# Kernel tuning notes

Hardware: AMD Instinct MI355X
Metric: run time of the kernel (lower is better)

The kernel has to match this reference:

```python
import jax, jax.numpy as jnp
import numpy as np

N_EMBD = 1024
N_HEAD = 16
EPS = 1e-5


def setup_inputs() -> dict:
    key = jax.random.key(0)
    ks = jax.random.split(key, 12)
    C = N_EMBD
    s = 1.0 / np.sqrt(C)
    s4 = 1.0 / np.sqrt(4 * C)
    return {
        "x": jax.random.normal(ks[0], (2, 2048, C), jnp.float32),
        # attention projections (stored as [in, out])
        "wq": jax.random.normal(ks[1], (C, C), jnp.float32) * s,
        "bq": jnp.zeros((C,), jnp.float32),
        "wk": jax.random.normal(ks[2], (C, C), jnp.float32) * s,
        "bk": jnp.zeros((C,), jnp.float32),
        "wv": jax.random.normal(ks[3], (C, C), jnp.float32) * s,
        "bv": jnp.zeros((C,), jnp.float32),
        # layernorms
        "ln1_w": jnp.ones((C,), jnp.float32),
        "ln1_b": jnp.zeros((C,), jnp.float32),
        "ln2_w": jnp.ones((C,), jnp.float32),
        "ln2_b": jnp.zeros((C,), jnp.float32),
        # MLP
        "w_fc": jax.random.normal(ks[4], (C, 4 * C), jnp.float32) * s,
        "b_fc": jnp.zeros((4 * C,), jnp.float32),
        "w_proj": jax.random.normal(ks[5], (4 * C, C), jnp.float32) * s4,
        "b_proj": jnp.zeros((C,), jnp.float32),
    }


def _layer_norm(x, w, b):
    mu = jnp.mean(x, axis=-1, keepdims=True)
    var = jnp.var(x, axis=-1, keepdims=True)
    return (x - mu) * jax.lax.rsqrt(var + EPS) * w + b


def _block(x, wq, bq, wk, bk, wv, bv, ln1_w, ln1_b, ln2_w, ln2_b,
           w_fc, b_fc, w_proj, b_proj):
    B, T, C = x.shape
    H, D = N_HEAD, C // N_HEAD
    h = _layer_norm(x, ln1_w, ln1_b)
    q = (h @ wq + bq).reshape(B, T, H, D).transpose(0, 2, 1, 3)  # [B,H,T,D]
    k = (h @ wk + bk).reshape(B, T, H, D).transpose(0, 2, 1, 3)
    v = (h @ wv + bv).reshape(B, T, H, D).transpose(0, 2, 1, 3)
    att = jnp.einsum("bhtd,bhsd->bhts", q, k) / np.sqrt(D)
    causal = jnp.tril(jnp.ones((T, T), bool))
    att = jnp.where(causal, att, -jnp.inf)
    att = jax.nn.softmax(att, axis=-1)
    y = jnp.einsum("bhts,bhsd->bhtd", att, v)
    y = y.transpose(0, 2, 1, 3).reshape(B, T, C)
    x = x + y
    h2 = _layer_norm(x, ln2_w, ln2_b)
    mlp = jax.nn.gelu(h2 @ w_fc + b_fc, approximate=False) @ w_proj + b_proj
    x = x + mlp
    return x, k, v


def reference(x, wq, bq, wk, bk, wv, bv, ln1_w, ln1_b, ln2_w, ln2_b,
              w_fc, b_fc, w_proj, b_proj):
    return _block(x, wq, bq, wk, bk, wv, bv, ln1_w, ln1_b, ln2_w, ln2_b,
                  w_fc, b_fc, w_proj, b_proj)
```

## Files before the change

### kernel.cpp

```cpp
#include <hip/hip_runtime.h>
#include <hip/hip_bf16.h>


#define T_SEQ 2048
#define C_DIM 1024
#define HEADS 16
#define HD    64

typedef __attribute__((ext_vector_type(8))) short s16x8;
typedef __attribute__((ext_vector_type(4))) short s16x4;
typedef __attribute__((ext_vector_type(4))) float f32x4;

__device__ __forceinline__ short f2bf(float f) {
    union { __hip_bfloat16 h; short s; } u;
    u.h = __float2bfloat16(f);
    return u.s;
}
__device__ __forceinline__ float bf2f(short s) {
    union { float f; unsigned u; } u;
    u.u = ((unsigned)(unsigned short)s) << 16;
    return u.f;
}

__device__ __forceinline__ void gload16(const void* g, void* l) {
    __builtin_amdgcn_global_load_lds(
        (const __attribute__((address_space(1))) void*)g,
        (__attribute__((address_space(3))) void*)l, 16, 0, 0);
}
#define VMCNT0 asm volatile("s_waitcnt vmcnt(0)" ::: "memory")
#define PRIO1  __builtin_amdgcn_s_setprio(1)
#define PRIO0  __builtin_amdgcn_s_setprio(0)

__global__ __launch_bounds__(256) void prep_kernel(
    const float* __restrict__ wq, const float* __restrict__ wk, const float* __restrict__ wv,
    const float* __restrict__ wfc, const float* __restrict__ wpr,
    short* __restrict__ wqkvt, short* __restrict__ wfct, short* __restrict__ wprt,
    const float* __restrict__ x, const float* __restrict__ ln1w, const float* __restrict__ ln1b,
    short* __restrict__ hb) {
    int b = blockIdx.x, tid = threadIdx.x;
    if (b < 11264) {
        const float* W; short* Wt; int K, N, n0, k0;
        if (b < 3072) {
            int which = b >> 10, sub = b & 1023;
            W = (which == 0) ? wq : ((which == 1) ? wk : wv);
            Wt = wqkvt + which * 1024 * 1024;
            K = 1024; N = 1024;
            n0 = (sub & 31) * 32; k0 = (sub >> 5) * 32;
        } else if (b < 7168) {
            int sub = b - 3072;
            W = wfc; Wt = wfct; K = 1024; N = 4096;
            n0 = (sub & 127) * 32; k0 = (sub >> 7) * 32;
        } else {
            int sub = b - 7168;
            W = wpr; Wt = wprt; K = 4096; N = 1024;
            n0 = (sub & 31) * 32; k0 = (sub >> 5) * 32;
        }
        __shared__ float t[32][33];
        int ty = tid >> 3, tx = tid & 7;
        float4 v = *(const float4*)&W[(size_t)(k0 + ty) * N + n0 + tx * 4];
        t[ty][tx * 4 + 0] = v.x; t[ty][tx * 4 + 1] = v.y;
        t[ty][tx * 4 + 2] = v.z; t[ty][tx * 4 + 3] = v.w;
        __syncthreads();
        int r = tid >> 3, c = tid & 7;
        s16x4 o;
#pragma unroll
        for (int j = 0; j < 4; j++) o[j] = f2bf(t[c * 4 + j][r]);
        *(s16x4*)&Wt[(size_t)(n0 + r) * K + k0 + c * 4] = o;
    } else {
        int row = b - 11264;
        float4 v = ((const float4*)(x + (size_t)row * C_DIM))[tid];
        float s  = v.x + v.y + v.z + v.w;
        float sq = v.x * v.x + v.y * v.y + v.z * v.z + v.w * v.w;
#pragma unroll
        for (int off = 32; off > 0; off >>= 1) {
            s  += __shfl_down(s, off, 64);
            sq += __shfl_down(sq, off, 64);
        }
        __shared__ float rs[4], rq[4];
        int wv2 = tid >> 6, ln = tid & 63;
        if (ln == 0) { rs[wv2] = s; rq[wv2] = sq; }
        __syncthreads();
        s = rs[0] + rs[1] + rs[2] + rs[3];
        sq = rq[0] + rq[1] + rq[2] + rq[3];
        float mean = s * (1.f / C_DIM);
        float rstd = rsqrtf(sq * (1.f / C_DIM) - mean * mean + 1e-5f);
        float4 wv4 = ((const float4*)ln1w)[tid];
        float4 bv4 = ((const float4*)ln1b)[tid];
        s16x4 o;
        o[0] = f2bf((v.x - mean) * rstd * wv4.x + bv4.x);
        o[1] = f2bf((v.y - mean) * rstd * wv4.y + bv4.y);
        o[2] = f2bf((v.z - mean) * rstd * wv4.z + bv4.z);
        o[3] = f2bf((v.w - mean) * rstd * wv4.w + bv4.w);
        *(s16x4*)(hb + (size_t)row * C_DIM + tid * 4) = o;
    }
}

__global__ __launch_bounds__(256) void resln_kernel(
    const float* __restrict__ x, const float* __restrict__ y,
    const float* __restrict__ w, const float* __restrict__ b,
    const float* __restrict__ bproj,
    short* __restrict__ out, float* __restrict__ xout) {
    int row = blockIdx.x, tid = threadIdx.x;
    float4 vx = ((const float4*)(x + row * C_DIM))[tid];
    float4 vy = ((const float4*)(y + row * C_DIM))[tid];
    float4 v;
    v.x = vx.x + vy.x; v.y = vx.y + vy.y; v.z = vx.z + vy.z; v.w = vx.w + vy.w;
    float4 bp = ((const float4*)bproj)[tid];
    float4 xo;
    xo.x = v.x + bp.x; xo.y = v.y + bp.y; xo.z = v.z + bp.z; xo.w = v.w + bp.w;
    ((float4*)(xout + row * C_DIM))[tid] = xo;
    float s  = v.x + v.y + v.z + v.w;
    float sq = v.x * v.x + v.y * v.y + v.z * v.z + v.w * v.w;
#pragma unroll
    for (int off = 32; off > 0; off >>= 1) {
        s  += __shfl_down(s, off, 64);
        sq += __shfl_down(sq, off, 64);
    }
    __shared__ float rs[4], rq[4];
    int wv = tid >> 6, ln = tid & 63;
    if (ln == 0) { rs[wv] = s; rq[wv] = sq; }
    __syncthreads();
    s = rs[0] + rs[1] + rs[2] + rs[3];
    sq = rq[0] + rq[1] + rq[2] + rq[3];
    float mean = s * (1.f / C_DIM);
    float rstd = rsqrtf(sq * (1.f / C_DIM) - mean * mean + 1e-5f);
    float4 wv4 = ((const float4*)w)[tid];
    float4 bv4 = ((const float4*)b)[tid];
    s16x4 o;
    o[0] = f2bf((v.x - mean) * rstd * wv4.x + bv4.x);
    o[1] = f2bf((v.y - mean) * rstd * wv4.y + bv4.y);
    o[2] = f2bf((v.z - mean) * rstd * wv4.z + bv4.z);
    o[3] = f2bf((v.w - mean) * rstd * wv4.w + bv4.w);
    *(s16x4*)(out + row * C_DIM + tid * 4) = o;
}

__global__ __launch_bounds__(256) void reduce_kernel(
    const short* __restrict__ p, float* __restrict__ xout) {
    size_t i = (size_t)blockIdx.x * 256 + threadIdx.x;
    float4 a = ((const float4*)xout)[i];
#pragma unroll
    for (int c = 0; c < 4; c++) {
        s16x4 v = ((const s16x4*)(p + (size_t)c * 4194304))[i];
        a.x += bf2f(v[0]); a.y += bf2f(v[1]); a.z += bf2f(v[2]); a.w += bf2f(v[3]);
    }
    ((float4*)xout)[i] = a;
}

template<int MODE>
__global__ __launch_bounds__(256, 3) void gemm97(
    const short* __restrict__ A, const short* __restrict__ Bt,
    int K, int LDA, int N,
    const float* __restrict__ b0, const float* __restrict__ b1, const float* __restrict__ b2,
    short* __restrict__ os0, short* __restrict__ os1, short* __restrict__ os2,
    float* __restrict__ of0) {
    __shared__ short As[128 * 64];
    __shared__ short Bs[128 * 64];
    const int tid = threadIdx.x;
    const int wv = tid >> 6, lane = tid & 63, g = lane >> 4, r4 = lane & 15;
    const int wr = wv >> 1, wc = wv & 1;
    const int lr = lane >> 3, lc = lane & 7, sc = lc ^ lr;

    const int nwg = gridDim.x * gridDim.y;
    const int bid = blockIdx.y * gridDim.x + blockIdx.x;
    const int swz = (bid & 7) * (nwg >> 3) + (bid >> 3);
    const int m0 = (swz % gridDim.x) * 128;
    const int yy = swz / gridDim.x;
    int n0, kch;
    if constexpr (MODE == 2) {
        kch = yy >> 3;
        n0 = (yy & 7) * 128;
    } else {
        kch = 0;
        n0 = yy * 128;
    }
    const size_t kbase = (size_t)kch * K;
    const size_t aoff = (size_t)m0 * LDA + kbase + sc * 8;
    const size_t boff = (size_t)n0 * LDA + kbase + sc * 8;

    const f32x4 zero4 = {0.f, 0.f, 0.f, 0.f};
    f32x4 acc[4][4];
#pragma unroll
    for (int i = 0; i < 4; i++)
#pragma unroll
        for (int j = 0; j < 4; j++) acc[i][j] = zero4;

    auto stage = [&](int t1) {
#pragma unroll
        for (int j = 0; j < 4; j++) {
            int rg = wv * 4 + j;
            gload16(A  + aoff + (size_t)(rg * 8 + lr) * LDA + (size_t)t1 * 64, &As[rg * 512]);
            gload16(Bt + boff + (size_t)(rg * 8 + lr) * LDA + (size_t)t1 * 64, &Bs[rg * 512]);
        }
    };

    stage(0);
    VMCNT0;
    __syncthreads();

    const int NT = K >> 6;
    for (int t = 0; t < NT; ++t) {
#pragma unroll
        for (int kk = 0; kk < 2; kk++) {
            s16x8 af[4], bfr[4];
#pragma unroll
            for (int mf = 0; mf < 4; mf++) {
                int row = wr * 64 + mf * 16 + r4;
                af[mf] = *(const s16x8*)((const char*)As +
                          ((row * 128 + kk * 64 + g * 16) ^ ((row & 7) << 4)));
            }
#pragma unroll
            for (int nf = 0; nf < 4; nf++) {
                int row = wc * 64 + nf * 16 + r4;
                bfr[nf] = *(const s16x8*)((const char*)Bs +
                           ((row * 128 + kk * 64 + g * 16) ^ ((row & 7) << 4)));
            }
#pragma unroll
            for (int mf = 0; mf < 4; mf++)
#pragma unroll
                for (int nf = 0; nf < 4; nf++)
                    acc[mf][nf] = __builtin_amdgcn_mfma_f32_16x16x32_bf16(
                        af[mf], bfr[nf], acc[mf][nf], 0, 0, 0);
        }
        __syncthreads();
        if (t + 1 < NT) stage(t + 1);
        VMCNT0;
        __syncthreads();
    }

#pragma unroll
    for (int mf = 0; mf < 4; mf++) {
#pragma unroll
        for (int nf = 0; nf < 4; nf++) {
            int n = n0 + wc * 64 + nf * 16 + r4;
            int mB = m0 + wr * 64 + mf * 16 + 4 * g;
            if constexpr (MODE == 0) {
                int sel = n >> 10, nn = n & 1023;
                const float* bp = (sel == 0) ? b0 : ((sel == 1) ? b1 : b2);
                float bias = bp[nn];
                int h = nn >> 6, d = nn & 63;
                int bb2 = mB >> 11, tt = mB & 2047;
                size_t qz = ((size_t)(bb2 * HEADS + h) * T_SEQ + tt) * HD + d;
                if (sel == 0) {
#pragma unroll
                    for (int r = 0; r < 4; r++) os0[qz + (size_t)r * HD] = f2bf(acc[mf][nf][r] + bias);
                } else if (sel == 1) {
#pragma unroll
                    for (int r = 0; r < 4; r++) {
                        float val = acc[mf][nf][r] + bias;
                        os1[qz + (size_t)r * HD] = f2bf(val);
                        of0[qz + (size_t)r * HD] = val;
                    }
                } else {
                    s16x4 vp;
#pragma unroll
                    for (int r = 0; r < 4; r++) {
                        float val = acc[mf][nf][r] + bias;
                        of0[4194304 + qz + (size_t)r * HD] = val;
                        vp[r] = f2bf(val);
                    }
                    *(s16x4*)&os2[((size_t)(bb2 * HEADS + h) * HD + d) * T_SEQ + tt] = vp;
                }
            } else if constexpr (MODE == 1) {
                float bias = b0[n];
#pragma unroll
                for (int r = 0; r < 4; r++) {
                    float val = acc[mf][nf][r] + bias;
                    val = 0.5f * val * (1.f + erff(val * 0.70710678118f));
                    os0[(size_t)(mB + r) * N + n] = f2bf(val);
                }
            } else {
#pragma unroll
                for (int r = 0; r < 4; r++)
                    os0[(size_t)kch * 4194304 + (size_t)(mB + r) * N + n] = f2bf(acc[mf][nf][r]);
            }
        }
    }
}

__global__ __launch_bounds__(256) void attn_kernel(
    const short* __restrict__ qb, const short* __restrict__ kb,
    const short* __restrict__ vtb, float* __restrict__ y) {
    __shared__ short Ks[2][64 * 64];
    __shared__ short Vs[2][64 * 64];
    __shared__ short Ps[4][16 * 64];
    int bx = blockIdx.x, bh = blockIdx.y;
    int tid = threadIdx.x, w = tid >> 6, lane = tid & 63, g = lane >> 4, r4 = lane & 15;
    int lr = lane >> 3, lc = lane & 7, sc = lc ^ lr;
    const float S2 = 0.125f * 1.44269504089f;
    const f32x4 zero4 = {0.f, 0.f, 0.f, 0.f};

    for (int ph = 0; ph < 2; ++ph) {
        int qtr = ph ? bx : (31 - bx);
        int qbase = qtr * 64;
        int nst = qtr + 1;

        const short* Qp = qb + ((size_t)bh * T_SEQ + qbase + w * 16 + r4) * HD;
        s16x8 qf0 = *(const s16x8*)&Qp[g * 8];
        s16x8 qf1 = *(const s16x8*)&Qp[32 + g * 8];

        f32x4 yacc[4];
#pragma unroll
        for (int ni = 0; ni < 4; ni++) yacc[ni] = zero4;
        float mrun = -1e30f, lrun = 0.f;

#pragma unroll
        for (int j = 0; j < 2; j++) {
            int rw = (w * 2 + j) * 8 + lr;
            gload16(kb  + ((size_t)bh * T_SEQ + rw) * HD + sc * 8, &Ks[0][(w * 2 + j) * 512]);
            gload16(vtb + ((size_t)bh * HD + rw) * T_SEQ + sc * 8, &Vs[0][(w * 2 + j) * 512]);
        }
        VMCNT0;
        __syncthreads();

        for (int st = 0; st < nst; ++st) {
            int cur = st & 1;
            int s0 = st * 64;
            if (st + 1 < nst) {
#pragma unroll
                for (int j = 0; j < 2; j++) {
                    int rw = (w * 2 + j) * 8 + lr;
                    gload16(kb  + ((size_t)bh * T_SEQ + s0 + 64 + rw) * HD + sc * 8,
                            &Ks[cur ^ 1][(w * 2 + j) * 512]);
                    gload16(vtb + ((size_t)bh * HD + rw) * T_SEQ + s0 + 64 + sc * 8,
                            &Vs[cur ^ 1][(w * 2 + j) * 512]);
                }
            }
            f32x4 sacc[4];
#pragma unroll
            for (int sb = 0; sb < 4; sb++) sacc[sb] = zero4;
            PRIO1;
#pragma unroll
            for (int kk = 0; kk < 2; kk++) {
                s16x8 qf = (kk == 0) ? qf0 : qf1;
#pragma unroll
                for (int sb = 0; sb < 4; sb++) {
                    int srow = sb * 16 + r4;
                    s16x8 kf = *(const s16x8*)((const char*)&Ks[cur][0] +
                                ((srow * 128 + kk * 64 + g * 16) ^ ((r4 & 7) << 4)));
                    sacc[sb] = __builtin_amdgcn_mfma_f32_16x16x32_bf16(kf, qf, sacc[sb], 0, 0, 0);
                }
            }
            PRIO0;
            bool diag = (st == qtr);
            float p[4][4];
            float mx = -1e30f;
#pragma unroll
            for (int sb = 0; sb < 4; sb++)
#pragma unroll
                for (int r = 0; r < 4; r++) {
                    float v = sacc[sb][r] * S2;
                    if (diag) {
                        int kv = s0 + sb * 16 + 4 * g + r;
                        int qg = qbase + w * 16 + r4;
                        if (kv > qg) v = -1e30f;
                    }
                    p[sb][r] = v;
                    mx = fmaxf(mx, v);
                }
            mx = fmaxf(mx, __shfl_xor(mx, 16, 64));
            mx = fmaxf(mx, __shfl_xor(mx, 32, 64));
            if (!__all(mx <= mrun + 8.f)) {
                float mnew = fmaxf(mrun, mx);
                float alpha = exp2f(mrun - mnew);
                float aC[4];
#pragma unroll
                for (int r = 0; r < 4; r++) aC[r] = __shfl(alpha, 4 * g + r, 64);
#pragma unroll
                for (int ni = 0; ni < 4; ni++)
#pragma unroll
                    for (int r = 0; r < 4; r++) yacc[ni][r] *= aC[r];
                lrun *= alpha;
                mrun = mnew;
            }
            float rsum = 0.f;
#pragma unroll
            for (int sb = 0; sb < 4; sb++)
#pragma unroll
                for (int r = 0; r < 4; r++) {
                    float e = exp2f(p[sb][r] - mrun);
                    p[sb][r] = e;
                    rsum += e;
                }
            rsum += __shfl_xor(rsum, 16, 64);
            rsum += __shfl_xor(rsum, 32, 64);
            lrun += rsum;
#pragma unroll
            for (int sb = 0; sb < 4; sb++) {
                s16x4 pk;
#pragma unroll
                for (int r = 0; r < 4; r++) pk[r] = f2bf(p[sb][r]);
                int off = (r4 * 128 + (sb * 16 + 4 * g) * 2) ^ ((r4 & 7) << 4);
                *(s16x4*)((char*)&Ps[w][0] + off) = pk;
            }
            PRIO1;
#pragma unroll
            for (int kk = 0; kk < 2; kk++) {
                s16x8 pf = *(const s16x8*)((const char*)&Ps[w][0] +
                            ((r4 * 128 + kk * 64 + g * 16) ^ ((r4 & 7) << 4)));
#pragma unroll
                for (int ni = 0; ni < 4; ni++) {
                    int vrow = ni * 16 + r4;
                    s16x8 vb = *(const s16x8*)((const char*)&Vs[cur][0] +
                                ((vrow * 128 + kk * 64 + g * 16) ^ ((r4 & 7) << 4)));
                    yacc[ni] = __builtin_amdgcn_mfma_f32_16x16x32_bf16(pf, vb, yacc[ni], 0, 0, 0);
                }
            }
            PRIO0;
            VMCNT0;
            __syncthreads();
        }
        float lC[4];
#pragma unroll
        for (int r = 0; r < 4; r++) lC[r] = __shfl(lrun, 4 * g + r, 64);
        int bb = bh >> 4, h = bh & 15;
#pragma unroll
        for (int ni = 0; ni < 4; ni++)
#pragma unroll
            for (int r = 0; r < 4; r++) {
                int q = qbase + w * 16 + 4 * g + r;
                y[((size_t)bb * T_SEQ + q) * C_DIM + h * HD + ni * 16 + r4] = yacc[ni][r] / lC[r];
            }
        __syncthreads();
    }
}

extern "C" void kernel_launch(void* const* d_in, const int* in_sizes, int n_in,
                              void* d_out, int out_size, void* d_ws, size_t ws_size,
                              hipStream_t stream) {
    (void)in_sizes; (void)n_in; (void)out_size; (void)ws_size;
    const float* x    = (const float*)d_in[0];
    const float* wq   = (const float*)d_in[1];
    const float* bq   = (const float*)d_in[2];
    const float* wk   = (const float*)d_in[3];
    const float* bk   = (const float*)d_in[4];
    const float* wvp  = (const float*)d_in[5];
    const float* bv   = (const float*)d_in[6];
    const float* ln1w = (const float*)d_in[7];
    const float* ln1b = (const float*)d_in[8];
    const float* ln2w = (const float*)d_in[9];
    const float* ln2b = (const float*)d_in[10];
    const float* wfc  = (const float*)d_in[11];
    const float* bfc  = (const float*)d_in[12];
    const float* wpr  = (const float*)d_in[13];
    const float* bpr  = (const float*)d_in[14];

    float* xout = (float*)d_out;
    float* kout = xout + 4194304;

    short* wqkvt = (short*)d_ws;
    short* wfct  = wqkvt + 3072 * 1024;
    short* wprt  = wfct + 4096 * 1024;
    short* hb    = wprt + 1024 * 4096;
    short* qb    = hb + 4096 * 1024;
    short* kbuf  = qb + 4096 * 1024;
    short* vtb   = kbuf + 4096 * 1024;
    short* h2b   = vtb + 4096 * 1024;
    short* fcb   = h2b + 4096 * 1024;
    float* ybuf  = (float*)(fcb + 4096 * 4096);
    short* pbuf  = qb;

    prep_kernel<<<15360, 256, 0, stream>>>(wq, wk, wvp, wfc, wpr,
        wqkvt, wfct, wprt, x, ln1w, ln1b, hb);

    gemm97<0><<<dim3(32, 24), 256, 0, stream>>>(hb, wqkvt, 1024, 1024, 3072,
        bq, bk, bv, qb, kbuf, vtb, kout);

    attn_kernel<<<dim3(16, 32), 256, 0, stream>>>(qb, kbuf, vtb, ybuf);

    resln_kernel<<<4096, 256, 0, stream>>>(x, ybuf, ln2w, ln2b, bpr, h2b, xout);

    gemm97<1><<<dim3(32, 32), 256, 0, stream>>>(h2b, wfct, 1024, 1024, 4096,
        bfc, nullptr, nullptr, fcb, nullptr, nullptr, nullptr);

    gemm97<2><<<dim3(32, 32), 256, 0, stream>>>(fcb, wprt, 1024, 4096, 1024,
        nullptr, nullptr, nullptr, pbuf, nullptr, nullptr, nullptr);

    reduce_kernel<<<4096, 256, 0, stream>>>(pbuf, xout);
}
```

Measured before the change: 239.3 us.

## Switch GEMMs to 256x256 tiles with 512 threads and double-buffered LDS

Replaces the 128x128, 256-thread GEMM with a 256x256, 512-thread variant in which each wave computes 128x64 of the output, raising operand reuse per LDS load. LDS is double-buffered: the next k-tile is prefetched while MFMAs run on the current one, which removes one barrier and the explicit vmcnt wait per iteration. MFMA blocks are also wrapped in priority hints. In exchange, grids shrink to 192 and 256 workgroups at one block per CU, which may leave CUs idle, and the kernel now needs 128KB of LDS.

```diff
diff --git a/kernel.cpp b/kernel.cpp
--- a/kernel.cpp
+++ b/kernel.cpp
@@ -147,92 +147,96 @@
 }
 
 template<int MODE>
-__global__ __launch_bounds__(256, 3) void gemm97(
+__global__ __launch_bounds__(512, 1) void gemm2p(
     const short* __restrict__ A, const short* __restrict__ Bt,
     int K, int LDA, int N,
     const float* __restrict__ b0, const float* __restrict__ b1, const float* __restrict__ b2,
     short* __restrict__ os0, short* __restrict__ os1, short* __restrict__ os2,
     float* __restrict__ of0) {
-    __shared__ short As[128 * 64];
-    __shared__ short Bs[128 * 64];
+    constexpr int MFR = 8, NFR = 4;
+
+    __shared__ short As[2][256 * 64];
+    __shared__ short Bs[2][256 * 64];
+
     const int tid = threadIdx.x;
     const int wv = tid >> 6, lane = tid & 63, g = lane >> 4, r4 = lane & 15;
-    const int wr = wv >> 1, wc = wv & 1;
+    const int wm = wv >> 2, wn = wv & 3;
     const int lr = lane >> 3, lc = lane & 7, sc = lc ^ lr;
 
     const int nwg = gridDim.x * gridDim.y;
     const int bid = blockIdx.y * gridDim.x + blockIdx.x;
     const int swz = (bid & 7) * (nwg >> 3) + (bid >> 3);
-    const int m0 = (swz % gridDim.x) * 128;
+    const int m0 = (swz % gridDim.x) * 256;
     const int yy = swz / gridDim.x;
     int n0, kch;
     if constexpr (MODE == 2) {
-        kch = yy >> 3;
-        n0 = (yy & 7) * 128;
+        kch = yy >> 2;
+        n0 = (yy & 3) * 256;
     } else {
         kch = 0;
-        n0 = yy * 128;
+        n0 = yy * 256;
     }
     const size_t kbase = (size_t)kch * K;
     const size_t aoff = (size_t)m0 * LDA + kbase + sc * 8;
     const size_t boff = (size_t)n0 * LDA + kbase + sc * 8;
 
     const f32x4 zero4 = {0.f, 0.f, 0.f, 0.f};
-    f32x4 acc[4][4];
-#pragma unroll
-    for (int i = 0; i < 4; i++)
-#pragma unroll
-        for (int j = 0; j < 4; j++) acc[i][j] = zero4;
-
-    auto stage = [&](int t1) {
+    f32x4 acc[MFR][NFR];
+#pragma unroll
+    for (int i = 0; i < MFR; i++)
+#pragma unroll
+        for (int j = 0; j < NFR; j++) acc[i][j] = zero4;
+
+    auto stage = [&](int bb, int t1) {
 #pragma unroll
         for (int j = 0; j < 4; j++) {
-            int rg = wv * 4 + j;
-            gload16(A  + aoff + (size_t)(rg * 8 + lr) * LDA + (size_t)t1 * 64, &As[rg * 512]);
-            gload16(Bt + boff + (size_t)(rg * 8 + lr) * LDA + (size_t)t1 * 64, &Bs[rg * 512]);
+            int rbase = j * 64 + wv * 8;
+            gload16(A  + aoff + (size_t)(rbase + lr) * LDA + (size_t)t1 * 64, &As[bb][rbase * 64]);
+            gload16(Bt + boff + (size_t)(rbase + lr) * LDA + (size_t)t1 * 64, &Bs[bb][rbase * 64]);
         }
     };
 
-    stage(0);
-    VMCNT0;
+    stage(0, 0);
     __syncthreads();
 
     const int NT = K >> 6;
+    int cur = 0;
     for (int t = 0; t < NT; ++t) {
+        if (t + 1 < NT) stage(cur ^ 1, t + 1);
+        const char* Ac = (const char*)&As[cur][0];
+        const char* Bc = (const char*)&Bs[cur][0];
 #pragma unroll
         for (int kk = 0; kk < 2; kk++) {
-            s16x8 af[4], bfr[4];
-#pragma unroll
-            for (int mf = 0; mf < 4; mf++) {
-                int row = wr * 64 + mf * 16 + r4;
-                af[mf] = *(const s16x8*)((const char*)As +
-                          ((row * 128 + kk * 64 + g * 16) ^ ((row & 7) << 4)));
-            }
-#pragma unroll
-            for (int nf = 0; nf < 4; nf++) {
-                int row = wc * 64 + nf * 16 + r4;
-                bfr[nf] = *(const s16x8*)((const char*)Bs +
-                           ((row * 128 + kk * 64 + g * 16) ^ ((row & 7) << 4)));
-            }
-#pragma unroll
-            for (int mf = 0; mf < 4; mf++)
-#pragma unroll
-                for (int nf = 0; nf < 4; nf++)
+            s16x8 aF[MFR], bF[NFR];
+#pragma unroll
+            for (int mf = 0; mf < MFR; mf++) {
+                int row = wm * 128 + mf * 16 + r4;
+                aF[mf] = *(const s16x8*)(Ac + ((row * 128 + kk * 64 + g * 16) ^ ((row & 7) << 4)));
+            }
+#pragma unroll
+            for (int nf = 0; nf < NFR; nf++) {
+                int row = wn * 64 + nf * 16 + r4;
+                bF[nf] = *(const s16x8*)(Bc + ((row * 128 + kk * 64 + g * 16) ^ ((row & 7) << 4)));
+            }
+            PRIO1;
+#pragma unroll
+            for (int mf = 0; mf < MFR; mf++)
+#pragma unroll
+                for (int nf = 0; nf < NFR; nf++)
                     acc[mf][nf] = __builtin_amdgcn_mfma_f32_16x16x32_bf16(
-                        af[mf], bfr[nf], acc[mf][nf], 0, 0, 0);
+                        aF[mf], bF[nf], acc[mf][nf], 0, 0, 0);
+            PRIO0;
         }
         __syncthreads();
-        if (t + 1 < NT) stage(t + 1);
-        VMCNT0;
-        __syncthreads();
-    }
-
-#pragma unroll
-    for (int mf = 0; mf < 4; mf++) {
-#pragma unroll
-        for (int nf = 0; nf < 4; nf++) {
-            int n = n0 + wc * 64 + nf * 16 + r4;
-            int mB = m0 + wr * 64 + mf * 16 + 4 * g;
+        cur ^= 1;
+    }
+
+#pragma unroll
+    for (int mf = 0; mf < MFR; mf++) {
+#pragma unroll
+        for (int nf = 0; nf < NFR; nf++) {
+            int n = n0 + wn * 64 + nf * 16 + r4;
+            int mB = m0 + wm * 128 + mf * 16 + 4 * g;
             if constexpr (MODE == 0) {
                 int sel = n >> 10, nn = n & 1023;
                 const float* bp = (sel == 0) ? b0 : ((sel == 1) ? b1 : b2);
@@ -462,17 +466,17 @@
     prep_kernel<<<15360, 256, 0, stream>>>(wq, wk, wvp, wfc, wpr,
         wqkvt, wfct, wprt, x, ln1w, ln1b, hb);
 
-    gemm97<0><<<dim3(32, 24), 256, 0, stream>>>(hb, wqkvt, 1024, 1024, 3072,
+    gemm2p<0><<<dim3(16, 12), 512, 0, stream>>>(hb, wqkvt, 1024, 1024, 3072,
         bq, bk, bv, qb, kbuf, vtb, kout);
 
     attn_kernel<<<dim3(16, 32), 256, 0, stream>>>(qb, kbuf, vtb, ybuf);
 
     resln_kernel<<<4096, 256, 0, stream>>>(x, ybuf, ln2w, ln2b, bpr, h2b, xout);
 
-    gemm97<1><<<dim3(32, 32), 256, 0, stream>>>(h2b, wfct, 1024, 1024, 4096,
+    gemm2p<1><<<dim3(16, 16), 512, 0, stream>>>(h2b, wfct, 1024, 1024, 4096,
         bfc, nullptr, nullptr, fcb, nullptr, nullptr, nullptr);
 
-    gemm97<2><<<dim3(32, 32), 256, 0, stream>>>(fcb, wprt, 1024, 4096, 1024,
+    gemm2p<2><<<dim3(16, 16), 512, 0, stream>>>(fcb, wprt, 1024, 4096, 1024,
         nullptr, nullptr, nullptr, pbuf, nullptr, nullptr, nullptr);
 
     reduce_kernel<<<4096, 256, 0, stream>>>(pbuf, xout);
```

Measured after the change: 241.3 us. Within noise of the previous version (+0.8%).
